# Optimization experiments

Hardware: AMD Instinct MI355X
Metric: run time of the kernel (lower is better)

## Reference

```python
import jax, jax.numpy as jnp
import numpy as np

VOCAB = 1276   # medical-code vocab (one_hot depth for word)
AGE_DEPTH = 91 # one_hot depth for age


def setup_inputs() -> dict:
    key = jax.random.key(0)
    k1, k2, k3 = jax.random.split(key, 3)
    B, S, BAG, D = 64, 128, 40, 768
    word = jax.random.randint(k1, (B, S, BAG), 0, VOCAB)
    age = jax.random.randint(k2, (B, S), 0, AGE_DEPTH)
    W = jax.random.normal(k3, (VOCAB + AGE_DEPTH, D), dtype=jnp.float32) * 0.02
    b = jnp.zeros((D,), dtype=jnp.float32)
    return {"word": word, "age": age, "W": W, "b": b}


def reference(word, age, W, b):
    # word: [B, S, BAG] int codes; age: [B, S] int.
    B, S, BAG = word.shape
    # Multi-hot count-sum: equivalent to reduce_sum(one_hot(word, VOCAB), axis=-2)
    # but computed via scatter-add, avoiding the dense [B,S,BAG,VOCAB] tensor.
    flat = word.reshape(B * S, BAG)
    offs = jnp.arange(B * S, dtype=word.dtype)[:, None] * VOCAB
    counts = (
        jnp.zeros((B * S * VOCAB,), jnp.float32)
        .at[(flat + offs).ravel()]
        .add(1.0)
        .reshape(B, S, VOCAB)
    )
    year = jax.nn.one_hot(age, AGE_DEPTH, dtype=jnp.float32)  # [B, S, 91]
    x = jnp.concatenate([counts, year], axis=-1)              # [B, S, 1367]
    return x @ W + b                                          # [B, S, 768]
```

## Files before the change

kernel.cpp:

```cpp
#include <hip/hip_runtime.h>
#include <hip/hip_fp16.h>

constexpr int BAG       = 40;
constexpr int D         = 768;
constexpr int VOCAB     = 1276;
constexpr int AGE_DEPTH = 91;
constexpr int WROWS     = VOCAB + AGE_DEPTH;

typedef float fx4 __attribute__((ext_vector_type(4)));

__device__ __forceinline__ __half2 u2h(uint u) {
    union { uint u; __half2 h; } v; v.u = u; return v.h;
}

__global__ __launch_bounds__(256) void convert_w_f16(
    const float* __restrict__ W, ushort* __restrict__ Wh, int n)
{
    const int i = (blockIdx.x * 256 + threadIdx.x) * 8;
    if (i + 8 > n) return;
    const float4 a = *reinterpret_cast<const float4*>(W + i);
    const float4 b = *reinterpret_cast<const float4*>(W + i + 4);
    const float v[8] = {a.x, a.y, a.z, a.w, b.x, b.y, b.z, b.w};
    ushort r[8];
    #pragma unroll
    for (int k = 0; k < 8; ++k) {
        __half h = __float2half(v[k]);
        r[k] = *reinterpret_cast<ushort*>(&h);
    }
    uint4 packed;
    packed.x = (uint)r[0] | ((uint)r[1] << 16);
    packed.y = (uint)r[2] | ((uint)r[3] << 16);
    packed.z = (uint)r[4] | ((uint)r[5] << 16);
    packed.w = (uint)r[6] | ((uint)r[7] << 16);
    *reinterpret_cast<uint4*>(Wh + i) = packed;
}

__global__ __launch_bounds__(192, 6) void embedbag_f16_kernel(
    const int* __restrict__ word,
    const int* __restrict__ age,
    const __half* __restrict__ Wh,
    const float* __restrict__ bias,
    float* __restrict__ out)
{
    const int tid  = threadIdx.x;
    const int sub  = tid / 96;
    const int lane = tid - sub * 96;
    const int row  = blockIdx.x * 2 + sub;
    const int c    = lane * 8;

    const int* __restrict__ wrow = word + row * BAG;
    const __half* __restrict__ wp = Wh + c;

    const int aidx = VOCAB + age[row];

    __half2 acc0 = u2h(0u), acc1 = u2h(0u), acc2 = u2h(0u), acc3 = u2h(0u);

    int idx[8];
    {
        const int4 q0 = *reinterpret_cast<const int4*>(wrow);
        const int4 q1 = *reinterpret_cast<const int4*>(wrow + 4);
        idx[0]=q0.x; idx[1]=q0.y; idx[2]=q0.z; idx[3]=q0.w;
        idx[4]=q1.x; idx[5]=q1.y; idx[6]=q1.z; idx[7]=q1.w;
    }

    #pragma unroll
    for (int kb = 0; kb < 5; ++kb) {
        uint4 g[8];
        #pragma unroll
        for (int u = 0; u < 8; ++u)
            g[u] = *reinterpret_cast<const uint4*>(wp + (size_t)idx[u] * D);

        int nxt[8];
        if (kb < 4) {
            const int4 q0 = *reinterpret_cast<const int4*>(wrow + 8 * kb + 8);
            const int4 q1 = *reinterpret_cast<const int4*>(wrow + 8 * kb + 12);
            nxt[0]=q0.x; nxt[1]=q0.y; nxt[2]=q0.z; nxt[3]=q0.w;
            nxt[4]=q1.x; nxt[5]=q1.y; nxt[6]=q1.z; nxt[7]=q1.w;
        }

        #pragma unroll
        for (int u = 0; u < 8; ++u) {
            acc0 = __hadd2(acc0, u2h(g[u].x));
            acc1 = __hadd2(acc1, u2h(g[u].y));
            acc2 = __hadd2(acc2, u2h(g[u].z));
            acc3 = __hadd2(acc3, u2h(g[u].w));
        }

        if (kb < 4) {
            #pragma unroll
            for (int u = 0; u < 8; ++u) idx[u] = nxt[u];
        }
    }

    {
        const uint4 g = *reinterpret_cast<const uint4*>(wp + (size_t)aidx * D);
        acc0 = __hadd2(acc0, u2h(g.x));
        acc1 = __hadd2(acc1, u2h(g.y));
        acc2 = __hadd2(acc2, u2h(g.z));
        acc3 = __hadd2(acc3, u2h(g.w));
    }

    const float4 b0 = *reinterpret_cast<const float4*>(bias + c);
    const float4 b1 = *reinterpret_cast<const float4*>(bias + c + 4);
    fx4 o0 = { b0.x + __low2float(acc0), b0.y + __high2float(acc0),
               b0.z + __low2float(acc1), b0.w + __high2float(acc1) };
    fx4 o1 = { b1.x + __low2float(acc2), b1.y + __high2float(acc2),
               b1.z + __low2float(acc3), b1.w + __high2float(acc3) };
    float* op = out + (size_t)row * D + c;
    __builtin_nontemporal_store(o0, reinterpret_cast<fx4*>(op));
    __builtin_nontemporal_store(o1, reinterpret_cast<fx4*>(op + 4));
}

__global__ __launch_bounds__(192) void embedbag_f32_kernel(
    const int* __restrict__ word, const int* __restrict__ age,
    const float* __restrict__ W, const float* __restrict__ bias,
    float* __restrict__ out)
{
    const int row = blockIdx.x;
    const int c   = threadIdx.x * 4;

    float4 acc = *reinterpret_cast<const float4*>(&bias[c]);
    const int* __restrict__ wrow = word + row * BAG;

    #pragma unroll 8
    for (int j = 0; j < BAG; ++j) {
        const int idx = wrow[j];
        const float4 v = *reinterpret_cast<const float4*>(&W[(size_t)idx * D + c]);
        acc.x += v.x; acc.y += v.y; acc.z += v.z; acc.w += v.w;
    }
    {
        const int idx = VOCAB + age[row];
        const float4 v = *reinterpret_cast<const float4*>(&W[(size_t)idx * D + c]);
        acc.x += v.x; acc.y += v.y; acc.z += v.z; acc.w += v.w;
    }
    *reinterpret_cast<float4*>(&out[(size_t)row * D + c]) = acc;
}

extern "C" void kernel_launch(void* const* d_in, const int* in_sizes, int n_in,
                              void* d_out, int out_size, void* d_ws, size_t ws_size,
                              hipStream_t stream) {
    const int* word   = (const int*)d_in[0];
    const int* age    = (const int*)d_in[1];
    const float* W    = (const float*)d_in[2];
    const float* bias = (const float*)d_in[3];
    float* out        = (float*)d_out;

    const int rows = in_sizes[1];

    const size_t need = (size_t)WROWS * D * sizeof(ushort);
    if (ws_size >= need) {
        ushort* Wh = (ushort*)d_ws;
        const int n = WROWS * D;
        convert_w_f16<<<(n / 8 + 255) / 256, 256, 0, stream>>>(W, Wh, n);
        embedbag_f16_kernel<<<rows / 2, 192, 0, stream>>>(
            word, age, (const __half*)Wh, bias, out);
    } else {
        embedbag_f32_kernel<<<rows, D / 4, 0, stream>>>(word, age, W, bias, out);
    }
}
```

Baseline: 33.16 us.

## Stage column slice of fp16 table in LDS and gather from shared memory

Each block now copies a 16-column slice of the whole fp16 weight table (all 1367 rows) into LDS, then serves 256 token rows whose bag gathers read from LDS instead of global/L2 memory. The grid is tiled over row blocks and column slices, with two threads per row covering 8 columns each. This trades scattered global gathers for a per-block LDS fill of about 44KB, which is redundant across row blocks, and relies on rows being a multiple of 256. Each row's word indices are also re-read once per column slice, and LDS gathers with random indices may hit bank conflicts.

```diff
diff --git a/kernel.cpp b/kernel.cpp
--- a/kernel.cpp
+++ b/kernel.cpp
@@ -7,10 +7,20 @@
 constexpr int AGE_DEPTH = 91;
 constexpr int WROWS     = VOCAB + AGE_DEPTH;
 
+constexpr int COLS = 16;
+constexpr int NSLC = D / COLS;
+constexpr int RPB  = 256;
+constexpr int TPB  = 512;
+constexpr int LDSU = 2 * WROWS;
+
 typedef float fx4 __attribute__((ext_vector_type(4)));
 
 __device__ __forceinline__ __half2 u2h(uint u) {
     union { uint u; __half2 h; } v; v.u = u; return v.h;
+}
+__device__ __forceinline__ ushort f2h(float f) {
+    __half h = __float2half(f);
+    return *reinterpret_cast<ushort*>(&h);
 }
 
 __global__ __launch_bounds__(256) void convert_w_f16(
@@ -20,55 +30,61 @@
     if (i + 8 > n) return;
     const float4 a = *reinterpret_cast<const float4*>(W + i);
     const float4 b = *reinterpret_cast<const float4*>(W + i + 4);
-    const float v[8] = {a.x, a.y, a.z, a.w, b.x, b.y, b.z, b.w};
-    ushort r[8];
-    #pragma unroll
-    for (int k = 0; k < 8; ++k) {
-        __half h = __float2half(v[k]);
-        r[k] = *reinterpret_cast<ushort*>(&h);
-    }
-    uint4 packed;
-    packed.x = (uint)r[0] | ((uint)r[1] << 16);
-    packed.y = (uint)r[2] | ((uint)r[3] << 16);
-    packed.z = (uint)r[4] | ((uint)r[5] << 16);
-    packed.w = (uint)r[6] | ((uint)r[7] << 16);
-    *reinterpret_cast<uint4*>(Wh + i) = packed;
+    uint4 p;
+    p.x = (uint)f2h(a.x) | ((uint)f2h(a.y) << 16);
+    p.y = (uint)f2h(a.z) | ((uint)f2h(a.w) << 16);
+    p.z = (uint)f2h(b.x) | ((uint)f2h(b.y) << 16);
+    p.w = (uint)f2h(b.z) | ((uint)f2h(b.w) << 16);
+    *reinterpret_cast<uint4*>(Wh + i) = p;
 }
 
-__global__ __launch_bounds__(192, 6) void embedbag_f16_kernel(
+__global__ __launch_bounds__(TPB) void embed_lds_kernel(
     const int* __restrict__ word,
     const int* __restrict__ age,
-    const __half* __restrict__ Wh,
+    const ushort* __restrict__ Wh,
     const float* __restrict__ bias,
     float* __restrict__ out)
 {
-    const int tid  = threadIdx.x;
-    const int sub  = tid / 96;
-    const int lane = tid - sub * 96;
-    const int row  = blockIdx.x * 2 + sub;
-    const int c    = lane * 8;
+    __shared__ uint4 lds4[LDSU];
+
+    const int rb = blockIdx.x;
+    const int c0 = blockIdx.y * COLS;
+
+    const int t     = threadIdx.x;
+    const int chunk = t & 1;
+    const int rloc  = t >> 1;
+    const int row   = rb * RPB + rloc;
 
     const int* __restrict__ wrow = word + row * BAG;
-    const __half* __restrict__ wp = Wh + c;
+
+    for (int s = t; s < LDSU; s += TPB) {
+        const int r = s >> 1;
+        const int u = s & 1;
+        lds4[u * WROWS + r] =
+            *reinterpret_cast<const uint4*>(Wh + (size_t)r * D + c0 + u * 8);
+    }
 
     const int aidx = VOCAB + age[row];
-
-    __half2 acc0 = u2h(0u), acc1 = u2h(0u), acc2 = u2h(0u), acc3 = u2h(0u);
-
-    int idx[8];
+    int cur[8];
     {
         const int4 q0 = *reinterpret_cast<const int4*>(wrow);
         const int4 q1 = *reinterpret_cast<const int4*>(wrow + 4);
-        idx[0]=q0.x; idx[1]=q0.y; idx[2]=q0.z; idx[3]=q0.w;
-        idx[4]=q1.x; idx[5]=q1.y; idx[6]=q1.z; idx[7]=q1.w;
+        cur[0]=q0.x; cur[1]=q0.y; cur[2]=q0.z; cur[3]=q0.w;
+        cur[4]=q1.x; cur[5]=q1.y; cur[6]=q1.z; cur[7]=q1.w;
     }
+
+    __syncthreads();
+
+    const uint4* __restrict__ lp = lds4 + chunk * WROWS;
+
+    __half2 a0 = u2h(0u), a1 = u2h(0u), a2 = u2h(0u), a3 = u2h(0u);
 
     #pragma unroll
     for (int kb = 0; kb < 5; ++kb) {
         uint4 g[8];
         #pragma unroll
         for (int u = 0; u < 8; ++u)
-            g[u] = *reinterpret_cast<const uint4*>(wp + (size_t)idx[u] * D);
+            g[u] = lp[cur[u]];
 
         int nxt[8];
         if (kb < 4) {
@@ -80,32 +96,33 @@
 
         #pragma unroll
         for (int u = 0; u < 8; ++u) {
-            acc0 = __hadd2(acc0, u2h(g[u].x));
-            acc1 = __hadd2(acc1, u2h(g[u].y));
-            acc2 = __hadd2(acc2, u2h(g[u].z));
-            acc3 = __hadd2(acc3, u2h(g[u].w));
+            a0 = __hadd2(a0, u2h(g[u].x));
+            a1 = __hadd2(a1, u2h(g[u].y));
+            a2 = __hadd2(a2, u2h(g[u].z));
+            a3 = __hadd2(a3, u2h(g[u].w));
         }
 
         if (kb < 4) {
             #pragma unroll
-            for (int u = 0; u < 8; ++u) idx[u] = nxt[u];
+            for (int u = 0; u < 8; ++u) cur[u] = nxt[u];
         }
     }
 
     {
-        const uint4 g = *reinterpret_cast<const uint4*>(wp + (size_t)aidx * D);
-        acc0 = __hadd2(acc0, u2h(g.x));
-        acc1 = __hadd2(acc1, u2h(g.y));
-        acc2 = __hadd2(acc2, u2h(g.z));
-        acc3 = __hadd2(acc3, u2h(g.w));
+        const uint4 g = lp[aidx];
+        a0 = __hadd2(a0, u2h(g.x));
+        a1 = __hadd2(a1, u2h(g.y));
+        a2 = __hadd2(a2, u2h(g.z));
+        a3 = __hadd2(a3, u2h(g.w));
     }
 
+    const int c = c0 + chunk * 8;
     const float4 b0 = *reinterpret_cast<const float4*>(bias + c);
     const float4 b1 = *reinterpret_cast<const float4*>(bias + c + 4);
-    fx4 o0 = { b0.x + __low2float(acc0), b0.y + __high2float(acc0),
-               b0.z + __low2float(acc1), b0.w + __high2float(acc1) };
-    fx4 o1 = { b1.x + __low2float(acc2), b1.y + __high2float(acc2),
-               b1.z + __low2float(acc3), b1.w + __high2float(acc3) };
+    fx4 o0 = { b0.x + __low2float(a0), b0.y + __high2float(a0),
+               b0.z + __low2float(a1), b0.w + __high2float(a1) };
+    fx4 o1 = { b1.x + __low2float(a2), b1.y + __high2float(a2),
+               b1.z + __low2float(a3), b1.w + __high2float(a3) };
     float* op = out + (size_t)row * D + c;
     __builtin_nontemporal_store(o0, reinterpret_cast<fx4*>(op));
     __builtin_nontemporal_store(o1, reinterpret_cast<fx4*>(op + 4));
@@ -148,12 +165,13 @@
     const int rows = in_sizes[1];
 
     const size_t need = (size_t)WROWS * D * sizeof(ushort);
-    if (ws_size >= need) {
+    if (rows % RPB == 0 && ws_size >= need) {
         ushort* Wh = (ushort*)d_ws;
         const int n = WROWS * D;
         convert_w_f16<<<(n / 8 + 255) / 256, 256, 0, stream>>>(W, Wh, n);
-        embedbag_f16_kernel<<<rows / 2, 192, 0, stream>>>(
-            word, age, (const __half*)Wh, bias, out);
+        dim3 grid(rows / RPB, NSLC);
+        embed_lds_kernel<<<grid, TPB, 0, stream>>>(
+            word, age, (const ushort*)Wh, bias, out);
     } else {
         embedbag_f32_kernel<<<rows, D / 4, 0, stream>>>(word, age, W, bias, out);
     }
```

New measurement: 31.62 us. 1.05x faster.
